# Kernel tuning notes

Hardware: AMD Instinct MI355X
Metric: run time of the kernel (lower is better)

Reference implementation:

```python
import jax, jax.numpy as jnp
import numpy as np

D_IN = 1024
D_OUT = 1024
NUM_HEADS = 16
HEAD_DIM = D_OUT // NUM_HEADS


def setup_inputs() -> dict:
    key = jax.random.key(0)
    ks = jax.random.split(key, 6)
    scale = 0.02
    x = jax.random.normal(ks[0], (2, 2048, D_IN), dtype=jnp.float32)
    Wq = jax.random.normal(ks[1], (D_IN, D_OUT), dtype=jnp.float32) * scale
    Wk = jax.random.normal(ks[2], (D_IN, D_OUT), dtype=jnp.float32) * scale
    Wv = jax.random.normal(ks[3], (D_IN, D_OUT), dtype=jnp.float32) * scale
    Wo = jax.random.normal(ks[4], (D_OUT, D_OUT), dtype=jnp.float32) * scale
    bo = jax.random.normal(ks[5], (D_OUT,), dtype=jnp.float32) * scale
    return {"x": x, "Wq": Wq, "Wk": Wk, "Wv": Wv, "Wo": Wo, "bo": bo}


def reference(x, Wq, Wk, Wv, Wo, bo):
    b, T, _ = x.shape
    h, dh = NUM_HEADS, HEAD_DIM
    # QKV projections (no bias), split heads: [b,T,d_out] -> [b,h,T,dh]
    q = (x @ Wq).reshape(b, T, h, dh).transpose(0, 2, 1, 3)
    k = (x @ Wk).reshape(b, T, h, dh).transpose(0, 2, 1, 3)
    v = (x @ Wv).reshape(b, T, h, dh).transpose(0, 2, 1, 3)
    # scaled dot-product scores with causal mask
    scores = jnp.einsum("bhqd,bhkd->bhqk", q, k) / jnp.sqrt(jnp.float32(dh))
    causal = jnp.tril(jnp.ones((T, T), dtype=bool))  # True = allowed
    scores = jnp.where(causal, scores, -jnp.inf)
    attn = jax.nn.softmax(scores, axis=-1)
    # dropout p=0.0 -> identity
    ctx = jnp.einsum("bhqk,bhkd->bhqd", attn, v)
    ctx = ctx.transpose(0, 2, 1, 3).reshape(b, T, h * dh)
    return ctx @ Wo + bo
```

## Files before the change

kernel.cpp:

```cpp
#include <hip/hip_runtime.h>

typedef __attribute__((ext_vector_type(8)))  __bf16 bf16x8;
typedef __attribute__((ext_vector_type(4)))  __bf16 bf16x4;
typedef __attribute__((ext_vector_type(4)))  float  f32x4;
typedef __attribute__((ext_vector_type(16))) float  f32x16;
typedef __attribute__((ext_vector_type(4)))  int    i32x4;

static constexpr int TSEQ    = 2048;
static constexpr int DMODEL  = 1024;
static constexpr int HD      = 64;
static constexpr int VSTRIDE = 2080;

#define AS1 __attribute__((address_space(1)))
#define AS3 __attribute__((address_space(3)))
#define SW(r) ((((r) & 12) >> 1) | ((r) & 1))

__global__ __launch_bounds__(256) void k_prep(const float* __restrict__ x,
    const float* __restrict__ w0, const float* __restrict__ w1,
    const float* __restrict__ w2, const float* __restrict__ w3,
    __bf16* __restrict__ xbf, __bf16* __restrict__ wt_all) {
  __shared__ float tile[32][33];
  const int blk = blockIdx.x;
  const int tid = threadIdx.x;
  if (blk < 4096) {
    size_t i = ((size_t)blk * 256 + tid) * 4;
    float4 v = *(const float4*)(x + i);
    bf16x4 o = { (__bf16)v.x, (__bf16)v.y, (__bf16)v.z, (__bf16)v.w };
    *(bf16x4*)(xbf + i) = o;
    return;
  }
  const int tz = blk - 4096;
  const int wi = tz >> 10;
  const int tl = tz & 1023;
  const int n0 = (tl & 31) * 32, k0 = (tl >> 5) * 32;
  const float* w = wi == 0 ? w0 : wi == 1 ? w1 : wi == 2 ? w2 : w3;
  __bf16* out = wt_all + (size_t)wi * DMODEL * DMODEL;
  const int tx = tid & 31, ty0 = (tid >> 5) * 4;
#pragma unroll
  for (int j = 0; j < 4; j++)
    tile[ty0 + j][tx] = w[(size_t)(k0 + ty0 + j) * DMODEL + n0 + tx];
  __syncthreads();
#pragma unroll
  for (int j = 0; j < 4; j++)
    out[(size_t)(n0 + ty0 + j) * DMODEL + k0 + tx] = (__bf16)tile[tx][ty0 + j];
}

__device__ __forceinline__ void gemm_mainloop(const __bf16* __restrict__ A,
                                              const __bf16* __restrict__ Bt,
                                              int bm, int bn,
                                              __bf16* At, __bf16* Bl,
                                              f32x4 acc[4][4]) {
  const int tid  = threadIdx.x;
  const int lane = tid & 63;
  const int l15  = lane & 15, quad = lane >> 4;
  const int wv   = tid >> 6;
  const int wm   = (wv >> 1) * 64, wn = (wv & 1) * 64;
  const int s0   = wv * 2;
  const int srow = lane >> 2;
  const int scol = (lane & 3) << 3;
  for (int k0 = 0; k0 < 1024; k0 += 32) {
    __syncthreads();
#pragma unroll
    for (int ss = 0; ss < 2; ss++) {
      const int s   = s0 + ss;
      const int row = s * 16 + srow;
      const __bf16* ga = A  + (size_t)(bm + row) * 1024 + k0 + scol;
      const __bf16* gb = Bt + (size_t)(bn + row) * 1024 + k0 + scol;
      __builtin_amdgcn_global_load_lds((const AS1 void*)ga,
                                       (AS3 void*)(At + s * 512), 16, 0, 0);
      __builtin_amdgcn_global_load_lds((const AS1 void*)gb,
                                       (AS3 void*)(Bl + s * 512), 16, 0, 0);
    }
    __syncthreads();
    bf16x8 af[4], bfr[4];
#pragma unroll
    for (int mt = 0; mt < 4; mt++)
      af[mt] = *(const bf16x8*)(At + (wm + mt * 16 + l15) * 32 + quad * 8);
#pragma unroll
    for (int nt = 0; nt < 4; nt++)
      bfr[nt] = *(const bf16x8*)(Bl + (wn + nt * 16 + l15) * 32 + quad * 8);
#pragma unroll
    for (int mt = 0; mt < 4; mt++)
#pragma unroll
      for (int nt = 0; nt < 4; nt++)
        acc[mt][nt] = __builtin_amdgcn_mfma_f32_16x16x32_bf16(
            af[mt], bfr[nt], acc[mt][nt], 0, 0, 0);
  }
}

__global__ __launch_bounds__(256) void k_gemm_qkv(const __bf16* __restrict__ xbf,
    const __bf16* __restrict__ wt_all, __bf16* __restrict__ qws,
    __bf16* __restrict__ kws, __bf16* __restrict__ vtws) {
  __shared__ __bf16 At[128 * 32];
  __shared__ __bf16 Bl[128 * 32];
  const int which = blockIdx.z;
  const __bf16* wt = wt_all + (size_t)which * DMODEL * DMODEL;
  const int bm = blockIdx.y * 128, bn = blockIdx.x * 128;
  f32x4 acc[4][4];
  const f32x4 z = {0.f, 0.f, 0.f, 0.f};
#pragma unroll
  for (int mt = 0; mt < 4; mt++)
#pragma unroll
    for (int nt = 0; nt < 4; nt++) acc[mt][nt] = z;
  gemm_mainloop(xbf, wt, bm, bn, At, Bl, acc);
  const int lane = threadIdx.x & 63;
  const int l15 = lane & 15, quad = lane >> 4;
  const int wv = threadIdx.x >> 6;
  const int wm = (wv >> 1) * 64, wn = (wv & 1) * 64;
#pragma unroll
  for (int mt = 0; mt < 4; mt++)
#pragma unroll
    for (int nt = 0; nt < 4; nt++)
#pragma unroll
      for (int r = 0; r < 4; r++) {
        int m = bm + wm + mt * 16 + quad * 4 + r;
        int n = bn + wn + nt * 16 + l15;
        int b = m >> 11, t = m & 2047;
        int h = n >> 6,  d = n & 63;
        int bh = b * 16 + h;
        float av = acc[mt][nt][r];
        if (which == 0)      qws[((size_t)bh * TSEQ + t) * HD + d] = (__bf16)(av * 0.18033688f);
        else if (which == 1) kws[((size_t)bh * TSEQ + t) * HD + d] = (__bf16)av;
        else                 vtws[((size_t)bh * HD + d) * VSTRIDE + t] = (__bf16)av;
      }
}

__global__ __launch_bounds__(256) void k_attn(const __bf16* __restrict__ qws,
    const __bf16* __restrict__ kws, const __bf16* __restrict__ vtws,
    __bf16* __restrict__ ctx) {
  const int bh = blockIdx.x & 31;
  const int tr = blockIdx.x >> 5;
  const int a  = (tr < 8) ? (15 - tr) : (tr - 8);
  const int tcnt = 2 * a + 2;
  const int tid = threadIdx.x;
  const int lane = tid & 63, wv = tid >> 6;
  const int l31 = lane & 31, hi = lane >> 5;
  const __bf16* qp = qws  + (size_t)bh * TSEQ * HD;
  const __bf16* kp = kws  + (size_t)bh * TSEQ * HD;
  const __bf16* vp = vtws + (size_t)bh * HD * VSTRIDE;
  const int b = bh >> 4, h = bh & 15;
  const int qbase = a * 128 + wv * 32;
  const int qg    = qbase + l31;

  __shared__ __align__(16) __bf16 kbuf[2][64 * 64];
  __shared__ __align__(16) __bf16 vbuf[2][64 * 64];

  const int sr = tid >> 3;
  const int c8 = tid & 7;

  bf16x8 aq[4];
#pragma unroll
  for (int s = 0; s < 4; s++)
    aq[s] = *(const bf16x8*)(qp + (size_t)qg * HD + s * 16 + hi * 8);

  bf16x8 kreg[2], vreg[2];
  kreg[0] = *(const bf16x8*)(kp + (size_t)sr * HD + c8 * 8);
  kreg[1] = *(const bf16x8*)(kp + (size_t)(sr + 32) * HD + c8 * 8);
  vreg[0] = *(const bf16x8*)(vp + (size_t)sr * VSTRIDE + c8 * 8);
  vreg[1] = *(const bf16x8*)(vp + (size_t)(sr + 32) * VSTRIDE + c8 * 8);
  *(bf16x8*)(kbuf[0] + sr * 64 + ((c8 ^ SW(sr)) << 3))             = kreg[0];
  *(bf16x8*)(kbuf[0] + (sr + 32) * 64 + ((c8 ^ SW(sr + 32)) << 3)) = kreg[1];
  *(bf16x8*)(vbuf[0] + sr * 64 + ((c8 ^ SW(sr)) << 3))             = vreg[0];
  *(bf16x8*)(vbuf[0] + (sr + 32) * 64 + ((c8 ^ SW(sr + 32)) << 3)) = vreg[1];
  __syncthreads();

  const f32x16 z16 = {0.f,0.f,0.f,0.f,0.f,0.f,0.f,0.f,0.f,0.f,0.f,0.f,0.f,0.f,0.f,0.f};
  float lpart = 0.f;
  f32x16 acc[2];
  acc[0] = z16; acc[1] = z16;

  for (int t = 0; t < tcnt; t++) {
    const int cur = t & 1;
    if (t + 1 < tcnt) {
      const int ktn = (t + 1) * 64;
      kreg[0] = *(const bf16x8*)(kp + (size_t)(ktn + sr) * HD + c8 * 8);
      kreg[1] = *(const bf16x8*)(kp + (size_t)(ktn + sr + 32) * HD + c8 * 8);
      vreg[0] = *(const bf16x8*)(vp + (size_t)sr * VSTRIDE + ktn + c8 * 8);
      vreg[1] = *(const bf16x8*)(vp + (size_t)(sr + 32) * VSTRIDE + ktn + c8 * 8);
    }

    const bool skipall = (t * 64) > (qbase + 31);
    if (!skipall) {
      const bool full = (t * 64 + 63) <= qbase;
      const __bf16* kb_ = kbuf[cur];
      const __bf16* vb_ = vbuf[cur];
#pragma unroll
      for (int kt = 0; kt < 2; kt++) {
        f32x16 s = z16;
#pragma unroll
        for (int ds = 0; ds < 4; ds++) {
          const int krow = kt * 32 + l31;
          bf16x8 ak = *(const bf16x8*)(kb_ + krow * 64 + (((ds * 2 + hi) ^ SW(krow)) << 3));
          s = __builtin_amdgcn_mfma_f32_32x32x16_bf16(ak, aq[ds], s, 0, 0, 0);
        }
        float pv[16];
        if (full) {
#pragma unroll
          for (int r = 0; r < 16; r++) {
            pv[r] = __builtin_amdgcn_exp2f(s[r]);
            lpart += pv[r];
          }
        } else {
#pragma unroll
          for (int r = 0; r < 16; r++) {
            const int kg = t * 64 + kt * 32 + (r & 3) + 8 * (r >> 2) + 4 * hi;
            float p = (kg <= qg) ? __builtin_amdgcn_exp2f(s[r]) : 0.f;
            pv[r] = p;
            lpart += p;
          }
        }
        int c[8];
#pragma unroll
        for (int j = 0; j < 8; j++) {
          int w;
          asm("v_cvt_pk_bf16_f32 %0, %1, %2" : "=v"(w) : "v"(pv[2 * j]), "v"(pv[2 * j + 1]));
          c[j] = w;
        }
        const int oc0 = __shfl_xor(c[0], 32, 64), oc1 = __shfl_xor(c[1], 32, 64);
        const int oc2 = __shfl_xor(c[2], 32, 64), oc3 = __shfl_xor(c[3], 32, 64);
        const int oc4 = __shfl_xor(c[4], 32, 64), oc5 = __shfl_xor(c[5], 32, 64);
        const int oc6 = __shfl_xor(c[6], 32, 64), oc7 = __shfl_xor(c[7], 32, 64);
        i32x4 w0 = { hi ? oc2 : c[0], hi ? oc3 : c[1], hi ? c[2] : oc0, hi ? c[3] : oc1 };
        i32x4 w1 = { hi ? oc6 : c[4], hi ? oc7 : c[5], hi ? c[6] : oc4, hi ? c[7] : oc5 };
        bf16x8 pa0 = __builtin_bit_cast(bf16x8, w0);
        bf16x8 pa1 = __builtin_bit_cast(bf16x8, w1);
#pragma unroll
        for (int dt = 0; dt < 2; dt++) {
          const int vrow = dt * 32 + l31;
          bf16x8 bv0 = *(const bf16x8*)(vb_ + vrow * 64 + (((kt * 4 + 0 + hi) ^ SW(vrow)) << 3));
          acc[dt] = __builtin_amdgcn_mfma_f32_32x32x16_bf16(pa0, bv0, acc[dt], 0, 0, 0);
          bf16x8 bv1 = *(const bf16x8*)(vb_ + vrow * 64 + (((kt * 4 + 2 + hi) ^ SW(vrow)) << 3));
          acc[dt] = __builtin_amdgcn_mfma_f32_32x32x16_bf16(pa1, bv1, acc[dt], 0, 0, 0);
        }
      }
    }

    if (t + 1 < tcnt) {
      const int nxt = cur ^ 1;
      *(bf16x8*)(kbuf[nxt] + sr * 64 + ((c8 ^ SW(sr)) << 3))             = kreg[0];
      *(bf16x8*)(kbuf[nxt] + (sr + 32) * 64 + ((c8 ^ SW(sr + 32)) << 3)) = kreg[1];
      *(bf16x8*)(vbuf[nxt] + sr * 64 + ((c8 ^ SW(sr)) << 3))             = vreg[0];
      *(bf16x8*)(vbuf[nxt] + (sr + 32) * 64 + ((c8 ^ SW(sr + 32)) << 3)) = vreg[1];
    }
    __syncthreads();
  }

  const float lfull = lpart + __shfl_xor(lpart, 32, 64);
#pragma unroll
  for (int r = 0; r < 16; r++) {
    const int ql = (r & 3) + 8 * (r >> 2) + 4 * hi;
    const float linv = 1.f / __shfl(lfull, ql, 64);
    const int qrow = qbase + ql;
#pragma unroll
    for (int dt = 0; dt < 2; dt++)
      ctx[((size_t)(b * TSEQ + qrow)) * DMODEL + h * 64 + dt * 32 + l31] =
          (__bf16)(acc[dt][r] * linv);
  }
}

__global__ __launch_bounds__(256) void k_gemm_out(const __bf16* __restrict__ ctx,
    const __bf16* __restrict__ wot, const float* __restrict__ bo,
    float* __restrict__ out) {
  __shared__ __bf16 At[128 * 32];
  __shared__ __bf16 Bl[128 * 32];
  const int bm = blockIdx.y * 128, bn = blockIdx.x * 128;
  f32x4 acc[4][4];
  const f32x4 z = {0.f, 0.f, 0.f, 0.f};
#pragma unroll
  for (int mt = 0; mt < 4; mt++)
#pragma unroll
    for (int nt = 0; nt < 4; nt++) acc[mt][nt] = z;
  gemm_mainloop(ctx, wot, bm, bn, At, Bl, acc);
  const int lane = threadIdx.x & 63;
  const int l15 = lane & 15, quad = lane >> 4;
  const int wv = threadIdx.x >> 6;
  const int wm = (wv >> 1) * 64, wn = (wv & 1) * 64;
#pragma unroll
  for (int mt = 0; mt < 4; mt++)
#pragma unroll
    for (int nt = 0; nt < 4; nt++)
#pragma unroll
      for (int r = 0; r < 4; r++) {
        int m = bm + wm + mt * 16 + quad * 4 + r;
        int n = bn + wn + nt * 16 + l15;
        out[(size_t)m * DMODEL + n] = acc[mt][nt][r] + bo[n];
      }
}

extern "C" void kernel_launch(void* const* d_in, const int* in_sizes, int n_in,
                              void* d_out, int out_size, void* d_ws, size_t ws_size,
                              hipStream_t stream) {
  const float* x  = (const float*)d_in[0];
  const float* Wq = (const float*)d_in[1];
  const float* Wk = (const float*)d_in[2];
  const float* Wv = (const float*)d_in[3];
  const float* Wo = (const float*)d_in[4];
  const float* bo = (const float*)d_in[5];
  float* out = (float*)d_out;

  __bf16* xbf  = (__bf16*)d_ws;
  __bf16* wt   = xbf  + (size_t)4096 * 1024;
  __bf16* qws  = wt   + (size_t)4 * 1024 * 1024;
  __bf16* kws  = qws  + (size_t)32 * 2048 * 64;
  __bf16* vtws = kws  + (size_t)32 * 2048 * 64;
  __bf16* ctx  = xbf;

  k_prep<<<8192, 256, 0, stream>>>(x, Wq, Wk, Wv, Wo, xbf, wt);
  k_gemm_qkv<<<dim3(8, 32, 3), 256, 0, stream>>>(xbf, wt, qws, kws, vtws);
  k_attn<<<512, 256, 0, stream>>>(qws, kws, vtws, ctx);
  k_gemm_out<<<dim3(8, 32), 256, 0, stream>>>(ctx, wt + (size_t)3 * 1024 * 1024, bo, out);
}
```

Measured before the change: 195.4 us.

## Split attention KV tiles across wave pairs with direct-to-LDS loads and reduction

Reorganizes the attention kernel so each wave handles 64 queries (two 32-row MFMA tiles) and waves are split by KV-tile parity, with results combined through an LDS exchange at the end. K/V staging now uses global_load_lds directly into a 4-deep LDS ring instead of a register round-trip, and the cross-half shuffle of P is replaced by split bf16x4 V reads. The aim is to reuse each K fragment across two query tiles, cut register staging and shuffles, and halve serial loop iterations. In exchange it uses twice the LDS, adds a final reduction, and needs more accumulator registers, which may lower occupancy.

```diff
diff --git a/kernel.cpp b/kernel.cpp
--- a/kernel.cpp
+++ b/kernel.cpp
@@ -131,130 +131,154 @@
   const int bh = blockIdx.x & 31;
   const int tr = blockIdx.x >> 5;
   const int a  = (tr < 8) ? (15 - tr) : (tr - 8);
-  const int tcnt = 2 * a + 2;
   const int tid = threadIdx.x;
-  const int lane = tid & 63, wv = tid >> 6;
+  const int lane = tid & 63;
+  const int wv = tid >> 6;
+  const int qh = wv & 1, kpar = wv >> 1;
   const int l31 = lane & 31, hi = lane >> 5;
   const __bf16* qp = qws  + (size_t)bh * TSEQ * HD;
   const __bf16* kp = kws  + (size_t)bh * TSEQ * HD;
   const __bf16* vp = vtws + (size_t)bh * HD * VSTRIDE;
   const int b = bh >> 4, h = bh & 15;
-  const int qbase = a * 128 + wv * 32;
-  const int qg    = qbase + l31;
-
-  __shared__ __align__(16) __bf16 kbuf[2][64 * 64];
-  __shared__ __align__(16) __bf16 vbuf[2][64 * 64];
-
-  const int sr = tid >> 3;
-  const int c8 = tid & 7;
-
-  bf16x8 aq[4];
-#pragma unroll
-  for (int s = 0; s < 4; s++)
-    aq[s] = *(const bf16x8*)(qp + (size_t)qg * HD + s * 16 + hi * 8);
-
-  bf16x8 kreg[2], vreg[2];
-  kreg[0] = *(const bf16x8*)(kp + (size_t)sr * HD + c8 * 8);
-  kreg[1] = *(const bf16x8*)(kp + (size_t)(sr + 32) * HD + c8 * 8);
-  vreg[0] = *(const bf16x8*)(vp + (size_t)sr * VSTRIDE + c8 * 8);
-  vreg[1] = *(const bf16x8*)(vp + (size_t)(sr + 32) * VSTRIDE + c8 * 8);
-  *(bf16x8*)(kbuf[0] + sr * 64 + ((c8 ^ SW(sr)) << 3))             = kreg[0];
-  *(bf16x8*)(kbuf[0] + (sr + 32) * 64 + ((c8 ^ SW(sr + 32)) << 3)) = kreg[1];
-  *(bf16x8*)(vbuf[0] + sr * 64 + ((c8 ^ SW(sr)) << 3))             = vreg[0];
-  *(bf16x8*)(vbuf[0] + (sr + 32) * 64 + ((c8 ^ SW(sr + 32)) << 3)) = vreg[1];
+  const int qbase = a * 128 + qh * 64;
+
+  __shared__ __align__(16) __bf16 kbuf[4][64 * 64];
+  __shared__ __align__(16) __bf16 vbuf[4][64 * 64];
+
+  const int srl = lane >> 3;
+  const int c8  = lane & 7;
+
+  auto stage = [&](int t) {
+    const int tb = t & 3;
+#pragma unroll
+    for (int g = 0; g < 4; g++) {
+      const int row = qh * 32 + g * 8 + srl;
+      const int swc = c8 ^ SW(row);
+      __builtin_amdgcn_global_load_lds(
+          (const AS1 void*)(kp + (size_t)(t * 64 + row) * HD + swc * 8),
+          (AS3 void*)(&kbuf[tb][(qh * 32 + g * 8) * 64]), 16, 0, 0);
+      __builtin_amdgcn_global_load_lds(
+          (const AS1 void*)(vp + (size_t)row * VSTRIDE + t * 64 + swc * 8),
+          (AS3 void*)(&vbuf[tb][(qh * 32 + g * 8) * 64]), 16, 0, 0);
+    }
+  };
+
+  bf16x8 aq[2][4];
+#pragma unroll
+  for (int m = 0; m < 2; m++)
+#pragma unroll
+    for (int ds = 0; ds < 4; ds++)
+      aq[m][ds] = *(const bf16x8*)(qp + (size_t)(qbase + m * 32 + l31) * HD + ds * 16 + hi * 8);
+
+  stage(kpar);
   __syncthreads();
 
   const f32x16 z16 = {0.f,0.f,0.f,0.f,0.f,0.f,0.f,0.f,0.f,0.f,0.f,0.f,0.f,0.f,0.f,0.f};
-  float lpart = 0.f;
-  f32x16 acc[2];
-  acc[0] = z16; acc[1] = z16;
-
-  for (int t = 0; t < tcnt; t++) {
-    const int cur = t & 1;
-    if (t + 1 < tcnt) {
-      const int ktn = (t + 1) * 64;
-      kreg[0] = *(const bf16x8*)(kp + (size_t)(ktn + sr) * HD + c8 * 8);
-      kreg[1] = *(const bf16x8*)(kp + (size_t)(ktn + sr + 32) * HD + c8 * 8);
-      vreg[0] = *(const bf16x8*)(vp + (size_t)sr * VSTRIDE + ktn + c8 * 8);
-      vreg[1] = *(const bf16x8*)(vp + (size_t)(sr + 32) * VSTRIDE + ktn + c8 * 8);
-    }
-
-    const bool skipall = (t * 64) > (qbase + 31);
-    if (!skipall) {
-      const bool full = (t * 64 + 63) <= qbase;
-      const __bf16* kb_ = kbuf[cur];
-      const __bf16* vb_ = vbuf[cur];
+  float lpart[2] = {0.f, 0.f};
+  f32x16 acc[2][2];
+  acc[0][0] = z16; acc[0][1] = z16; acc[1][0] = z16; acc[1][1] = z16;
+
+  for (int j = 0; j <= a; j++) {
+    const int t = 2 * j + kpar;
+    if (j < a) stage(t + 2);
+    if (t * 64 <= qbase + 63) {
+      const __bf16* kb_ = kbuf[t & 3];
+      const __bf16* vb_ = vbuf[t & 3];
 #pragma unroll
       for (int kt = 0; kt < 2; kt++) {
-        f32x16 s = z16;
-#pragma unroll
-        for (int ds = 0; ds < 4; ds++) {
-          const int krow = kt * 32 + l31;
-          bf16x8 ak = *(const bf16x8*)(kb_ + krow * 64 + (((ds * 2 + hi) ^ SW(krow)) << 3));
-          s = __builtin_amdgcn_mfma_f32_32x32x16_bf16(ak, aq[ds], s, 0, 0, 0);
+        const int kts = t * 64 + kt * 32;
+        const int krow = kt * 32 + l31;
+        bf16x8 ak[4];
+#pragma unroll
+        for (int ds = 0; ds < 4; ds++)
+          ak[ds] = *(const bf16x8*)(kb_ + krow * 64 + (((ds * 2 + hi) ^ SW(krow)) << 3));
+        bf16x8 pa[2][2];
+#pragma unroll
+        for (int m = 0; m < 2; m++) {
+          if (kts > qbase + m * 32 + 31) continue;
+          const int qg = qbase + m * 32 + l31;
+          f32x16 s = z16;
+#pragma unroll
+          for (int ds = 0; ds < 4; ds++)
+            s = __builtin_amdgcn_mfma_f32_32x32x16_bf16(ak[ds], aq[m][ds], s, 0, 0, 0);
+          float pvv[16];
+          if (kts + 31 <= qbase + m * 32) {
+#pragma unroll
+            for (int r = 0; r < 16; r++) {
+              pvv[r] = __builtin_amdgcn_exp2f(s[r]);
+              lpart[m] += pvv[r];
+            }
+          } else {
+#pragma unroll
+            for (int r = 0; r < 16; r++) {
+              const int kg = kts + (r & 3) + 8 * (r >> 2) + 4 * hi;
+              float p = (kg <= qg) ? __builtin_amdgcn_exp2f(s[r]) : 0.f;
+              pvv[r] = p;
+              lpart[m] += p;
+            }
+          }
+          int c[8];
+#pragma unroll
+          for (int jj = 0; jj < 8; jj++) {
+            int w;
+            asm("v_cvt_pk_bf16_f32 %0, %1, %2" : "=v"(w) : "v"(pvv[2 * jj]), "v"(pvv[2 * jj + 1]));
+            c[jj] = w;
+          }
+          i32x4 w0 = { c[0], c[1], c[2], c[3] };
+          i32x4 w1 = { c[4], c[5], c[6], c[7] };
+          pa[m][0] = __builtin_bit_cast(bf16x8, w0);
+          pa[m][1] = __builtin_bit_cast(bf16x8, w1);
         }
-        float pv[16];
-        if (full) {
-#pragma unroll
-          for (int r = 0; r < 16; r++) {
-            pv[r] = __builtin_amdgcn_exp2f(s[r]);
-            lpart += pv[r];
-          }
-        } else {
-#pragma unroll
-          for (int r = 0; r < 16; r++) {
-            const int kg = t * 64 + kt * 32 + (r & 3) + 8 * (r >> 2) + 4 * hi;
-            float p = (kg <= qg) ? __builtin_amdgcn_exp2f(s[r]) : 0.f;
-            pv[r] = p;
-            lpart += p;
-          }
-        }
-        int c[8];
-#pragma unroll
-        for (int j = 0; j < 8; j++) {
-          int w;
-          asm("v_cvt_pk_bf16_f32 %0, %1, %2" : "=v"(w) : "v"(pv[2 * j]), "v"(pv[2 * j + 1]));
-          c[j] = w;
-        }
-        const int oc0 = __shfl_xor(c[0], 32, 64), oc1 = __shfl_xor(c[1], 32, 64);
-        const int oc2 = __shfl_xor(c[2], 32, 64), oc3 = __shfl_xor(c[3], 32, 64);
-        const int oc4 = __shfl_xor(c[4], 32, 64), oc5 = __shfl_xor(c[5], 32, 64);
-        const int oc6 = __shfl_xor(c[6], 32, 64), oc7 = __shfl_xor(c[7], 32, 64);
-        i32x4 w0 = { hi ? oc2 : c[0], hi ? oc3 : c[1], hi ? c[2] : oc0, hi ? c[3] : oc1 };
-        i32x4 w1 = { hi ? oc6 : c[4], hi ? oc7 : c[5], hi ? c[6] : oc4, hi ? c[7] : oc5 };
-        bf16x8 pa0 = __builtin_bit_cast(bf16x8, w0);
-        bf16x8 pa1 = __builtin_bit_cast(bf16x8, w1);
 #pragma unroll
         for (int dt = 0; dt < 2; dt++) {
           const int vrow = dt * 32 + l31;
-          bf16x8 bv0 = *(const bf16x8*)(vb_ + vrow * 64 + (((kt * 4 + 0 + hi) ^ SW(vrow)) << 3));
-          acc[dt] = __builtin_amdgcn_mfma_f32_32x32x16_bf16(pa0, bv0, acc[dt], 0, 0, 0);
-          bf16x8 bv1 = *(const bf16x8*)(vb_ + vrow * 64 + (((kt * 4 + 2 + hi) ^ SW(vrow)) << 3));
-          acc[dt] = __builtin_amdgcn_mfma_f32_32x32x16_bf16(pa1, bv1, acc[dt], 0, 0, 0);
+#pragma unroll
+          for (int s2 = 0; s2 < 2; s2++) {
+            bf16x4 blo = *(const bf16x4*)(vb_ + vrow * 64 +
+                             (((kt * 4 + s2 * 2) ^ SW(vrow)) << 3) + 4 * hi);
+            bf16x4 bhi = *(const bf16x4*)(vb_ + vrow * 64 +
+                             (((kt * 4 + s2 * 2 + 1) ^ SW(vrow)) << 3) + 4 * hi);
+            bf16x8 bv = __builtin_shufflevector(blo, bhi, 0, 1, 2, 3, 4, 5, 6, 7);
+#pragma unroll
+            for (int m = 0; m < 2; m++) {
+              if (kts > qbase + m * 32 + 31) continue;
+              acc[m][dt] = __builtin_amdgcn_mfma_f32_32x32x16_bf16(pa[m][s2], bv, acc[m][dt], 0, 0, 0);
+            }
+          }
         }
       }
     }
-
-    if (t + 1 < tcnt) {
-      const int nxt = cur ^ 1;
-      *(bf16x8*)(kbuf[nxt] + sr * 64 + ((c8 ^ SW(sr)) << 3))             = kreg[0];
-      *(bf16x8*)(kbuf[nxt] + (sr + 32) * 64 + ((c8 ^ SW(sr + 32)) << 3)) = kreg[1];
-      *(bf16x8*)(vbuf[nxt] + sr * 64 + ((c8 ^ SW(sr)) << 3))             = vreg[0];
-      *(bf16x8*)(vbuf[nxt] + (sr + 32) * 64 + ((c8 ^ SW(sr + 32)) << 3)) = vreg[1];
+    __syncthreads();
+  }
+
+  float lf[2];
+#pragma unroll
+  for (int m = 0; m < 2; m++) lf[m] = lpart[m] + __shfl_xor(lpart[m], 32, 64);
+
+  float* exch = (float*)&kbuf[0][0];
+  float* lsm  = (float*)&vbuf[0][0];
+  const int give = kpar ^ 1;
+#pragma unroll
+  for (int m = 0; m < 2; m++) {
+#pragma unroll
+    for (int r = 0; r < 16; r++)
+      exch[((wv * 2 + m) * 16 + r) * 64 + lane] = acc[m][give][r];
+    lsm[(wv * 2 + m) * 64 + lane] = lf[m];
+  }
+  __syncthreads();
+  const int pwv = wv ^ 2;
+#pragma unroll
+  for (int m = 0; m < 2; m++) {
+    const float lfin = lf[m] + lsm[(pwv * 2 + m) * 64 + lane];
+#pragma unroll
+    for (int r = 0; r < 16; r++) {
+      const int ql = (r & 3) + 8 * (r >> 2) + 4 * hi;
+      const float den  = __shfl(lfin, ql, 64);
+      const float linv = __builtin_amdgcn_rcpf(den);
+      const float val  = (acc[m][kpar][r] + exch[((pwv * 2 + m) * 16 + r) * 64 + lane]) * linv;
+      const int qrow = qbase + m * 32 + ql;
+      ctx[((size_t)(b * TSEQ + qrow)) * DMODEL + h * 64 + kpar * 32 + l31] = (__bf16)val;
     }
-    __syncthreads();
-  }
-
-  const float lfull = lpart + __shfl_xor(lpart, 32, 64);
-#pragma unroll
-  for (int r = 0; r < 16; r++) {
-    const int ql = (r & 3) + 8 * (r >> 2) + 4 * hi;
-    const float linv = 1.f / __shfl(lfull, ql, 64);
-    const int qrow = qbase + ql;
-#pragma unroll
-    for (int dt = 0; dt < 2; dt++)
-      ctx[((size_t)(b * TSEQ + qrow)) * DMODEL + h * 64 + dt * 32 + l31] =
-          (__bf16)(acc[dt][r] * linv);
   }
 }
 
```

Measured after the change: 289.3 us. 1.48x slower.
